# Performance work log

Measured on AMD Instinct MI355X. Metric: run time of the kernel, lower is better.

Reference implementation:

```python
import jax, jax.numpy as jnp
import numpy as np

B, T, D = 16, 512, 384
MAX_LEN = 4096

def setup_inputs() -> dict:
    key = jax.random.key(0)
    k1, k2 = jax.random.split(key)
    encoder_out = jax.random.normal(k1, (B, T, D), dtype=jnp.float32)
    durations = jax.random.randint(k2, (B, T), 0, 8, dtype=jnp.int32)
    return {"encoder_out": encoder_out, "durations": durations, "max_len": MAX_LEN}

def _expand(encoder_out, durations, max_len):
    # Inclusive cumulative durations per sample: cum[b, t] = sum_{s<=t} dur[b, s]
    cum = jnp.cumsum(durations, axis=1)                     # [B, T]
    mel_lens = cum[:, -1]                                   # [B]
    pos = jnp.arange(max_len, dtype=cum.dtype)              # [L]
    # Output frame l belongs to the first token t with cum[t] > l.
    tok_idx = jax.vmap(lambda c: jnp.searchsorted(c, pos, side='right'))(cum)  # [B, L]
    tok_idx = jnp.clip(tok_idx, 0, durations.shape[1] - 1)
    expanded = jnp.take_along_axis(encoder_out, tok_idx[:, :, None], axis=1)   # [B, L, D]
    # Zero positions beyond each sample's total duration (matches zeros init + sequential fill).
    valid = pos[None, :] < jnp.minimum(mel_lens, max_len)[:, None]             # [B, L]
    expanded = jnp.where(valid[:, :, None], expanded, jnp.zeros((), expanded.dtype))
    return expanded, mel_lens

def reference(encoder_out, durations, max_len):
    return _expand(encoder_out, durations, max_len)
```

## Files before the change

### kernel.cpp

```cpp
#include <hip/hip_runtime.h>


#define LR_B       16
#define LR_T       512
#define LR_D4      96
#define LR_FRAMES  64
#define LR_THREADS 512

__global__ __launch_bounds__(LR_THREADS)
void lr_expand_kernel(const float4* __restrict__ enc,
                      const int*    __restrict__ dur,
                      float*        __restrict__ out,
                      int max_len) {
    const int b    = blockIdx.y;
    const int pos0 = blockIdx.x * LR_FRAMES;
    const int tid  = threadIdx.x;

    __shared__ int s_cum[LR_T];
    __shared__ int s_tok[LR_FRAMES];

    s_cum[tid] = dur[b * LR_T + tid];
    __syncthreads();
#pragma unroll
    for (int off = 1; off < LR_T; off <<= 1) {
        int v = (tid >= off) ? s_cum[tid - off] : 0;
        __syncthreads();
        s_cum[tid] += v;
        __syncthreads();
    }

    const int mel_raw = s_cum[LR_T - 1];
    const int mel     = min(mel_raw, max_len);

    if (blockIdx.x == 0 && tid == 0) {
        out[(size_t)LR_B * max_len * (LR_D4 * 4) + b] = (float)mel_raw;
    }

    if (tid < LR_FRAMES) {
        int pos = pos0 + tid;
        int lo = 0, hi = LR_T;
        while (lo < hi) {
            int mid = (lo + hi) >> 1;
            if (s_cum[mid] <= pos) lo = mid + 1; else hi = mid;
        }
        s_tok[tid] = min(lo, LR_T - 1);
    }
    __syncthreads();

    float4* out4 = (float4*)out;
    const size_t out_base = ((size_t)b * max_len + pos0) * LR_D4;
    const float4 zero4 = make_float4(0.f, 0.f, 0.f, 0.f);
#pragma unroll
    for (int it = 0; it < (LR_FRAMES * LR_D4) / LR_THREADS; ++it) {
        int j   = it * LR_THREADS + tid;
        int f   = j / LR_D4;
        int d4  = j - f * LR_D4;
        int pos = pos0 + f;
        if (pos >= max_len) continue;
        float4 val = zero4;
        if (pos < mel) {
            val = enc[(size_t)(b * LR_T + s_tok[f]) * LR_D4 + d4];
        }
        out4[out_base + (size_t)f * LR_D4 + d4] = val;
    }
}

extern "C" void kernel_launch(void* const* d_in, const int* in_sizes, int n_in,
                              void* d_out, int out_size, void* d_ws, size_t ws_size,
                              hipStream_t stream) {
    const float4* enc = (const float4*)d_in[0];
    const int*    dur = (const int*)d_in[1];
    float*        out = (float*)d_out;

    const int max_len = (out_size - LR_B) / (LR_B * LR_D4 * 4);

    dim3 grid((max_len + LR_FRAMES - 1) / LR_FRAMES, LR_B);
    lr_expand_kernel<<<grid, LR_THREADS, 0, stream>>>(enc, dur, out, max_len);
}
```

Baseline: 123.0 us.

## Split prefix scan into separate kernel and stream copies with nontemporal stores

Previously every block of the expand kernel recomputed the full 512-element prefix scan over durations. Now a small per-sample kernel computes the scan once and writes a token index per output frame (or -1 for padding) into workspace. A second kernel gathers encoder rows by those indices and writes them with nontemporal stores. This adds a kernel launch and a round trip of the token array through memory. The fused kernel is kept as a fallback when the workspace is too small.

```diff
diff --git a/kernel.cpp b/kernel.cpp
--- a/kernel.cpp
+++ b/kernel.cpp
@@ -4,14 +4,81 @@
 #define LR_B       16
 #define LR_T       512
 #define LR_D4      96
+
+typedef float f32x4 __attribute__((ext_vector_type(4)));
+
+__global__ __launch_bounds__(LR_T)
+void lr_scan_kernel(const int* __restrict__ dur,
+                    int*       __restrict__ tok,
+                    float*     __restrict__ mel_out,
+                    int max_len) {
+    const int b   = blockIdx.x;
+    const int tid = threadIdx.x;
+
+    __shared__ int s_cum[LR_T];
+    s_cum[tid] = dur[b * LR_T + tid];
+    __syncthreads();
+#pragma unroll
+    for (int off = 1; off < LR_T; off <<= 1) {
+        int v = (tid >= off) ? s_cum[tid - off] : 0;
+        __syncthreads();
+        s_cum[tid] += v;
+        __syncthreads();
+    }
+
+    const int mel_raw = s_cum[LR_T - 1];
+    const int mel     = min(mel_raw, max_len);
+    if (tid == 0) mel_out[b] = (float)mel_raw;
+
+    for (int pos = tid; pos < max_len; pos += LR_T) {
+        int t = -1;
+        if (pos < mel) {
+            int lo = 0, hi = LR_T;
+            while (lo < hi) {
+                int mid = (lo + hi) >> 1;
+                if (s_cum[mid] <= pos) lo = mid + 1; else hi = mid;
+            }
+            t = min(lo, LR_T - 1);
+        }
+        tok[b * max_len + pos] = t;
+    }
+}
+
+#define LR_CP_THREADS 384
+#define LR_CP_FRAMES  64
+
+__global__ __launch_bounds__(LR_CP_THREADS)
+void lr_copy_kernel(const f32x4* __restrict__ enc,
+                    const int*   __restrict__ tok,
+                    f32x4*       __restrict__ out4,
+                    int max_len) {
+    const int b   = blockIdx.y;
+    const int f0  = blockIdx.x * LR_CP_FRAMES;
+    const int d4  = threadIdx.x % LR_D4;
+    const int fs  = threadIdx.x / LR_D4;
+
+    const int*  tokb = tok + (size_t)b * max_len;
+    const f32x4 zero = {0.f, 0.f, 0.f, 0.f};
+    const size_t ob  = (size_t)b * max_len * LR_D4;
+    const size_t eb  = (size_t)b * LR_T * LR_D4;
+
+#pragma unroll
+    for (int i = 0; i < LR_CP_FRAMES / 4; ++i) {
+        const int f = f0 + i * 4 + fs;
+        const int t = tokb[f];
+        f32x4 v = zero;
+        if (t >= 0) v = enc[eb + (size_t)t * LR_D4 + d4];
+        __builtin_nontemporal_store(v, &out4[ob + (size_t)f * LR_D4 + d4]);
+    }
+}
+
 #define LR_FRAMES  64
 #define LR_THREADS 512
-
 __global__ __launch_bounds__(LR_THREADS)
-void lr_expand_kernel(const float4* __restrict__ enc,
-                      const int*    __restrict__ dur,
-                      float*        __restrict__ out,
-                      int max_len) {
+void lr_fused_kernel(const float4* __restrict__ enc,
+                     const int*    __restrict__ dur,
+                     float*        __restrict__ out,
+                     int max_len) {
     const int b    = blockIdx.y;
     const int pos0 = blockIdx.x * LR_FRAMES;
     const int tid  = threadIdx.x;
@@ -28,13 +95,10 @@
         s_cum[tid] += v;
         __syncthreads();
     }
-
     const int mel_raw = s_cum[LR_T - 1];
     const int mel     = min(mel_raw, max_len);
-
-    if (blockIdx.x == 0 && tid == 0) {
+    if (blockIdx.x == 0 && tid == 0)
         out[(size_t)LR_B * max_len * (LR_D4 * 4) + b] = (float)mel_raw;
-    }
 
     if (tid < LR_FRAMES) {
         int pos = pos0 + tid;
@@ -58,9 +122,7 @@
         int pos = pos0 + f;
         if (pos >= max_len) continue;
         float4 val = zero4;
-        if (pos < mel) {
-            val = enc[(size_t)(b * LR_T + s_tok[f]) * LR_D4 + d4];
-        }
+        if (pos < mel) val = enc[(size_t)(b * LR_T + s_tok[f]) * LR_D4 + d4];
         out4[out_base + (size_t)f * LR_D4 + d4] = val;
     }
 }
@@ -68,12 +130,24 @@
 extern "C" void kernel_launch(void* const* d_in, const int* in_sizes, int n_in,
                               void* d_out, int out_size, void* d_ws, size_t ws_size,
                               hipStream_t stream) {
-    const float4* enc = (const float4*)d_in[0];
-    const int*    dur = (const int*)d_in[1];
-    float*        out = (float*)d_out;
+    const int* dur = (const int*)d_in[1];
+    float*     out = (float*)d_out;
 
     const int max_len = (out_size - LR_B) / (LR_B * LR_D4 * 4);
+    const size_t tok_bytes = (size_t)LR_B * max_len * sizeof(int);
 
-    dim3 grid((max_len + LR_FRAMES - 1) / LR_FRAMES, LR_B);
-    lr_expand_kernel<<<grid, LR_THREADS, 0, stream>>>(enc, dur, out, max_len);
+    if (ws_size >= tok_bytes) {
+        int*   tok     = (int*)d_ws;
+        float* mel_out = out + (size_t)LR_B * max_len * (LR_D4 * 4);
+
+        lr_scan_kernel<<<LR_B, LR_T, 0, stream>>>(dur, tok, mel_out, max_len);
+
+        dim3 grid((max_len + LR_CP_FRAMES - 1) / LR_CP_FRAMES, LR_B);
+        lr_copy_kernel<<<grid, LR_CP_THREADS, 0, stream>>>(
+            (const f32x4*)d_in[0], tok, (f32x4*)out, max_len);
+    } else {
+        dim3 grid((max_len + LR_FRAMES - 1) / LR_FRAMES, LR_B);
+        lr_fused_kernel<<<grid, LR_THREADS, 0, stream>>>(
+            (const float4*)d_in[0], dur, out, max_len);
+    }
 }
```

Result: slower. 132.5 us (+7.7%).

## Replace block-wide scan with per-wavefront shuffle scan and nontemporal stores

Applied to the files above, without the earlier changes.

Each wavefront now computes the full 512-element duration prefix sum on its own, using vectorized loads, a serial 8-element partial sum and a 64-lane shuffle scan into a private shared segment. This removes the block-level Hillis-Steele scan and its many __syncthreads. Each wavefront handles 8 frames, gets token indices from lanes by shuffle, and writes output with nontemporal stores. Every wave repeats the scan (8x redundant), and nontemporal stores change cache behaviour.

```diff
diff --git a/kernel.cpp b/kernel.cpp
--- a/kernel.cpp
+++ b/kernel.cpp
@@ -1,79 +1,89 @@
 #include <hip/hip_runtime.h>
 
 
-#define LR_B       16
-#define LR_T       512
-#define LR_D4      96
-#define LR_FRAMES  64
-#define LR_THREADS 512
+#define LR_B   16
+#define LR_T   512
+#define LR_D4  96
 
-__global__ __launch_bounds__(LR_THREADS)
-void lr_expand_kernel(const float4* __restrict__ enc,
-                      const int*    __restrict__ dur,
-                      float*        __restrict__ out,
-                      int max_len) {
+typedef float f32x4 __attribute__((ext_vector_type(4)));
+typedef int   i32x4 __attribute__((ext_vector_type(4)));
+
+__global__ __launch_bounds__(512)
+void lr_kernel(const f32x4* __restrict__ enc,
+               const int*   __restrict__ dur,
+               f32x4*       __restrict__ out4,
+               float*       __restrict__ mel_out,
+               int max_len) {
     const int b    = blockIdx.y;
-    const int pos0 = blockIdx.x * LR_FRAMES;
+    const int f0   = blockIdx.x * 64;
     const int tid  = threadIdx.x;
+    const int lane = tid & 63;
+    const int wid  = tid >> 6;
 
-    __shared__ int s_cum[LR_T];
-    __shared__ int s_tok[LR_FRAMES];
+    __shared__ int s_cum[8][LR_T];
 
-    s_cum[tid] = dur[b * LR_T + tid];
-    __syncthreads();
+    const i32x4* durRow = (const i32x4*)(dur + b * LR_T);
+    i32x4 dA = durRow[lane * 2];
+    i32x4 dB = durRow[lane * 2 + 1];
+    int c0 = dA.x,      c1 = c0 + dA.y, c2 = c1 + dA.z, c3 = c2 + dA.w;
+    int c4 = c3 + dB.x, c5 = c4 + dB.y, c6 = c5 + dB.z, c7 = c6 + dB.w;
+    int v = c7;
 #pragma unroll
-    for (int off = 1; off < LR_T; off <<= 1) {
-        int v = (tid >= off) ? s_cum[tid - off] : 0;
-        __syncthreads();
-        s_cum[tid] += v;
-        __syncthreads();
+    for (int off = 1; off < 64; off <<= 1) {
+        int u = __shfl_up(v, off);
+        if (lane >= off) v += u;
+    }
+    const int base = v - c7;
+    int* seg = &s_cum[wid][0];
+    i32x4 wA = {c0 + base, c1 + base, c2 + base, c3 + base};
+    i32x4 wB = {c4 + base, c5 + base, c6 + base, c7 + base};
+    ((i32x4*)seg)[lane * 2]     = wA;
+    ((i32x4*)seg)[lane * 2 + 1] = wB;
+
+    const int mel_raw = __shfl(v, 63);
+    const int mel     = min(mel_raw, max_len);
+    if (blockIdx.x == 0 && tid == 0) mel_out[b] = (float)mel_raw;
+
+    int tok = -1;
+    {
+        const int pos = f0 + wid * 8 + lane;
+        if (lane < 8 && pos < mel) {
+            int lo = 0, hi = LR_T;
+            while (lo < hi) {
+                int mid = (lo + hi) >> 1;
+                if (seg[mid] <= pos) lo = mid + 1; else hi = mid;
+            }
+            tok = min(lo, LR_T - 1);
+        }
     }
 
-    const int mel_raw = s_cum[LR_T - 1];
-    const int mel     = min(mel_raw, max_len);
-
-    if (blockIdx.x == 0 && tid == 0) {
-        out[(size_t)LR_B * max_len * (LR_D4 * 4) + b] = (float)mel_raw;
-    }
-
-    if (tid < LR_FRAMES) {
-        int pos = pos0 + tid;
-        int lo = 0, hi = LR_T;
-        while (lo < hi) {
-            int mid = (lo + hi) >> 1;
-            if (s_cum[mid] <= pos) lo = mid + 1; else hi = mid;
-        }
-        s_tok[tid] = min(lo, LR_T - 1);
-    }
-    __syncthreads();
-
-    float4* out4 = (float4*)out;
-    const size_t out_base = ((size_t)b * max_len + pos0) * LR_D4;
-    const float4 zero4 = make_float4(0.f, 0.f, 0.f, 0.f);
+    const size_t eb = (size_t)b * LR_T * LR_D4;
+    const size_t ob = ((size_t)b * max_len + f0 + wid * 8) * LR_D4;
+    const int fbase = f0 + wid * 8;
+    const f32x4 zero = {0.f, 0.f, 0.f, 0.f};
 #pragma unroll
-    for (int it = 0; it < (LR_FRAMES * LR_D4) / LR_THREADS; ++it) {
-        int j   = it * LR_THREADS + tid;
-        int f   = j / LR_D4;
-        int d4  = j - f * LR_D4;
-        int pos = pos0 + f;
-        if (pos >= max_len) continue;
-        float4 val = zero4;
-        if (pos < mel) {
-            val = enc[(size_t)(b * LR_T + s_tok[f]) * LR_D4 + d4];
-        }
-        out4[out_base + (size_t)f * LR_D4 + d4] = val;
+    for (int i = 0; i < 12; ++i) {
+        const int e  = i * 64 + lane;
+        const int fl = e / LR_D4;
+        const int d4 = e - fl * LR_D4;
+        const int t  = __shfl(tok, fl);
+        f32x4 val = zero;
+        if (t >= 0) val = enc[eb + (size_t)t * LR_D4 + d4];
+        if (fbase + fl < max_len)
+            __builtin_nontemporal_store(val, &out4[ob + e]);
     }
 }
 
 extern "C" void kernel_launch(void* const* d_in, const int* in_sizes, int n_in,
                               void* d_out, int out_size, void* d_ws, size_t ws_size,
                               hipStream_t stream) {
-    const float4* enc = (const float4*)d_in[0];
-    const int*    dur = (const int*)d_in[1];
-    float*        out = (float*)d_out;
+    const f32x4* enc = (const f32x4*)d_in[0];
+    const int*   dur = (const int*)d_in[1];
+    float*       out = (float*)d_out;
 
     const int max_len = (out_size - LR_B) / (LR_B * LR_D4 * 4);
+    float* mel_out = out + (size_t)LR_B * max_len * (LR_D4 * 4);
 
-    dim3 grid((max_len + LR_FRAMES - 1) / LR_FRAMES, LR_B);
-    lr_expand_kernel<<<grid, LR_THREADS, 0, stream>>>(enc, dur, out, max_len);
+    dim3 grid((max_len + 63) / 64, LR_B);
+    lr_kernel<<<grid, 512, 0, stream>>>(enc, dur, (f32x4*)out, mel_out, max_len);
 }
```

Measured after the change: 129.6 us. 5.4% more time.
